# Kernel optimization log

Hardware: AMD Instinct MI355X
Metric: run time of the kernel (lower is better)

Reference implementation:

```python
import jax, jax.numpy as jnp
import numpy as np

N_NODES = 100000


def gcn_conv(x, edge_index, W, b, n_nodes):
    # PyG GCNConv: add self-loops, symmetric normalization D^-1/2 (A+I) D^-1/2, then XW + b
    xw = x @ W  # [N, out]
    loops = jnp.arange(n_nodes, dtype=edge_index.dtype)
    src = jnp.concatenate([edge_index[0], loops])  # [E+N]
    dst = jnp.concatenate([edge_index[1], loops])
    deg = jax.ops.segment_sum(jnp.ones_like(dst, dtype=xw.dtype), dst, num_segments=n_nodes)
    dinv = jnp.where(deg > 0, deg ** -0.5, 0.0).astype(xw.dtype)
    norm = dinv[src] * dinv[dst]  # [E+N]
    msgs = xw[src] * norm[:, None]  # gather source features, scale
    out = jax.ops.segment_sum(msgs, dst, num_segments=n_nodes)  # scatter-add at dst
    return out + b


def setup_inputs() -> dict:
    key = jax.random.key(0)
    k1, k2, k3, k4 = jax.random.split(key, 4)
    F_in, dim, n_cls, n_edges = 512, 32, 40, 3200000
    x = jax.random.normal(k1, (N_NODES, F_in), dtype=jnp.float32)
    edge_index = jax.random.randint(k2, (2, n_edges), 0, N_NODES, dtype=jnp.int64)
    W1 = jax.random.normal(k3, (F_in, dim), dtype=jnp.float32) * (1.0 / np.sqrt(F_in))
    b1 = jnp.zeros((dim,), dtype=jnp.float32)
    W2 = jax.random.normal(k4, (dim, n_cls), dtype=jnp.float32) * (1.0 / np.sqrt(dim))
    b2 = jnp.zeros((n_cls,), dtype=jnp.float32)
    return {"x": x, "edge_index": edge_index, "W1": W1, "b1": b1, "W2": W2, "b2": b2}


def reference(x, edge_index, W1, b1, W2, b2):
    h = jax.nn.relu(gcn_conv(x, edge_index, W1, b1, N_NODES))
    # F.dropout with training=False (eval) is identity
    logits = gcn_conv(h, edge_index, W2, b2, N_NODES)
    return jax.nn.log_softmax(logits, axis=1)
```

## Files before the change

### kernel.cpp

```cpp
#include <hip/hip_runtime.h>
#include <hip/hip_bf16.h>
#include <math.h>


#define DIM 32
#define NCLS 40
#define F_IN 512
#define BSH 8
#define EPB 8192
#define LMAX 9216

__device__ __forceinline__ unsigned int bf16rne(float x) {
    unsigned int u = __float_as_uint(x);
    return (u + 0x7fffu + ((u >> 16) & 1u)) >> 16;
}
__device__ __forceinline__ unsigned int packpair(float lo, float hi) {
    return bf16rne(lo) | (bf16rne(hi) << 16);
}
__device__ __forceinline__ void unpack8(uint4 u, float* f) {
    f[0] = __uint_as_float(u.x << 16);
    f[1] = __uint_as_float(u.x & 0xffff0000u);
    f[2] = __uint_as_float(u.y << 16);
    f[3] = __uint_as_float(u.y & 0xffff0000u);
    f[4] = __uint_as_float(u.z << 16);
    f[5] = __uint_as_float(u.z & 0xffff0000u);
    f[6] = __uint_as_float(u.w << 16);
    f[7] = __uint_as_float(u.w & 0xffff0000u);
}

__global__ __launch_bounds__(256) void hist_k(const int* __restrict__ dst,
                                              int* __restrict__ gh, int E, int nbk) {
    __shared__ int h[512];
    int tid = threadIdx.x;
    h[tid] = 0; h[tid + 256] = 0;
    __syncthreads();
    int base = blockIdx.x * EPB;
#pragma unroll 4
    for (int k = 0; k < EPB / 256; ++k) {
        int e = base + k * 256 + tid;
        if (e < E) atomicAdd(&h[dst[e] >> BSH], 1);
    }
    __syncthreads();
    if (h[tid]) atomicAdd(&gh[tid], h[tid]);
    if (h[tid + 256]) atomicAdd(&gh[tid + 256], h[tid + 256]);
}

__global__ __launch_bounds__(512) void scanb_k(const int* __restrict__ gh,
                                               int* __restrict__ bbase,
                                               int* __restrict__ gcur, int nbk) {
    __shared__ int sh[512];
    int t = threadIdx.x;
    int c = (t < nbk) ? gh[t] : 0;
    sh[t] = c;
    __syncthreads();
    for (int off = 1; off < 512; off <<= 1) {
        int v = sh[t];
        if (t >= off) v += sh[t - off];
        __syncthreads();
        sh[t] = v;
        __syncthreads();
    }
    int excl = sh[t] - c;
    if (t < nbk) { bbase[t] = excl; gcur[t] = excl; }
    if (t == 0) bbase[nbk] = sh[511];
}

__global__ __launch_bounds__(256) void part_k(const int* __restrict__ src,
                                              const int* __restrict__ dst,
                                              int* __restrict__ gcur,
                                              int* __restrict__ pairs, int E) {
    __shared__ int st[EPB];
    __shared__ int h[512];
    __shared__ int hb[512];
    int tid = threadIdx.x;
    h[tid] = 0; h[tid + 256] = 0;
    __syncthreads();
    int base = blockIdx.x * EPB;
#pragma unroll 4
    for (int k = 0; k < EPB / 256; ++k) {
        int e = base + k * 256 + tid;
        if (e < E) {
            int d = dst[e];
            st[k * 256 + tid] = d;
            atomicAdd(&h[d >> BSH], 1);
        }
    }
    __syncthreads();
    for (int b = tid; b < 512; b += 256) {
        int cnt = h[b];
        hb[b] = cnt ? atomicAdd(&gcur[b], cnt) : 0;
        h[b] = 0;
    }
    __syncthreads();
#pragma unroll 4
    for (int k = 0; k < EPB / 256; ++k) {
        int e = base + k * 256 + tid;
        if (e < E) {
            int d = st[k * 256 + tid];
            int b = d >> BSH;
            int r = atomicAdd(&h[b], 1);
            pairs[hb[b] + r] = ((d & 255) << 17) | src[e];
        }
    }
}

__global__ __launch_bounds__(256) void build_k(const int* __restrict__ pairs,
                                               const int* __restrict__ bbase,
                                               int* __restrict__ rowptr,
                                               int* __restrict__ csr,
                                               float* __restrict__ dinv,
                                               int n, int nbk, int E) {
    __shared__ int lcsr[LMAX];
    __shared__ int bins[256 * 17];
    __shared__ int cnt[256];
    __shared__ int sc[256];
    __shared__ int cur[256];
    int tid = threadIdx.x;
    int b = blockIdx.x;
    int lo = bbase[b], hi = bbase[b + 1];
    int cb = hi - lo; if (cb > LMAX) cb = LMAX;
    cnt[tid] = 0;
    __syncthreads();
    const int* Pb = pairs + lo;
    for (int i = tid; i < cb; i += 256)
        atomicAdd(&cnt[Pb[i] >> 17], 1);
    __syncthreads();
    int c = cnt[tid];
    sc[tid] = c;
    __syncthreads();
    for (int off = 1; off < 256; off <<= 1) {
        int v = sc[tid];
        if (tid >= off) v += sc[tid - off];
        __syncthreads();
        sc[tid] = v;
        __syncthreads();
    }
    int excl = sc[tid] - c;
    int v = (b << BSH) + tid;
    if (v < n) {
        rowptr[v] = lo + excl;
        dinv[v] = rsqrtf((float)(c + 1));
    }
    cur[tid] = excl;
    __syncthreads();
    for (int i = tid; i < cb; i += 256) {
        int p = Pb[i];
        int pos = atomicAdd(&cur[p >> 17], 1);
        lcsr[pos] = p & 0x1FFFF;
    }
    __syncthreads();
    {
        int* mb = &bins[tid * 17];
        int s = excl, e = excl + c;
#pragma unroll
        for (int k = 0; k < 16; ++k) mb[k] = 0;
        for (int i = s; i < e; ++i) ++mb[lcsr[i] >> 13];
        int run = s;
#pragma unroll
        for (int k = 0; k < 16; ++k) { int q = mb[k]; mb[k] = run; run += q; }
        for (int i = s; i < e; ++i) {
            int val = lcsr[i];
            int k = val >> 13;
            int pos = mb[k]++;
            csr[lo + pos] = val;
        }
    }
    if (b == 0 && tid == 0) rowptr[n] = E;
}

#define GR 128
__global__ __launch_bounds__(256) void gemm1_k(const float* __restrict__ x,
                                               const float* __restrict__ W1,
                                               const float* __restrict__ dinv,
                                               unsigned short* __restrict__ xwp, int n) {
    __shared__ float xs[32 * GR];
    __shared__ float ws[32 * 32];
    int tid = threadIdx.x;
    int base = blockIdx.x * GR;
    int rg = tid & 31;
    int cg = tid >> 5;
    float acc[4][4];
#pragma unroll
    for (int i = 0; i < 4; ++i)
#pragma unroll
        for (int j = 0; j < 4; ++j) acc[i][j] = 0.f;

    int lr = tid >> 1;
    int lq = tid & 1;
    int grow = base + lr;
    if (grow >= n) grow = n - 1;
    const float* xrow = x + (size_t)grow * F_IN;
    int wk = tid >> 3;
    int wc = tid & 7;

    for (int k0 = 0; k0 < F_IN; k0 += 32) {
        float4 a[4];
#pragma unroll
        for (int j = 0; j < 4; ++j)
            a[j] = *(const float4*)(xrow + k0 + lq * 16 + j * 4);
        float4 wv = *(const float4*)(W1 + (size_t)(k0 + wk) * DIM + wc * 4);
        __syncthreads();
#pragma unroll
        for (int j = 0; j < 4; ++j) {
            xs[(lq * 16 + j * 4 + 0) * GR + lr] = a[j].x;
            xs[(lq * 16 + j * 4 + 1) * GR + lr] = a[j].y;
            xs[(lq * 16 + j * 4 + 2) * GR + lr] = a[j].z;
            xs[(lq * 16 + j * 4 + 3) * GR + lr] = a[j].w;
        }
        *(float4*)&ws[wk * 32 + wc * 4] = wv;
        __syncthreads();
#pragma unroll 8
        for (int kk = 0; kk < 32; ++kk) {
            float4 xv = *(const float4*)&xs[kk * GR + rg * 4];
            float4 wv2 = *(const float4*)&ws[kk * 32 + cg * 4];
            acc[0][0] = fmaf(xv.x, wv2.x, acc[0][0]);
            acc[0][1] = fmaf(xv.x, wv2.y, acc[0][1]);
            acc[0][2] = fmaf(xv.x, wv2.z, acc[0][2]);
            acc[0][3] = fmaf(xv.x, wv2.w, acc[0][3]);
            acc[1][0] = fmaf(xv.y, wv2.x, acc[1][0]);
            acc[1][1] = fmaf(xv.y, wv2.y, acc[1][1]);
            acc[1][2] = fmaf(xv.y, wv2.z, acc[1][2]);
            acc[1][3] = fmaf(xv.y, wv2.w, acc[1][3]);
            acc[2][0] = fmaf(xv.z, wv2.x, acc[2][0]);
            acc[2][1] = fmaf(xv.z, wv2.y, acc[2][1]);
            acc[2][2] = fmaf(xv.z, wv2.z, acc[2][2]);
            acc[2][3] = fmaf(xv.z, wv2.w, acc[2][3]);
            acc[3][0] = fmaf(xv.w, wv2.x, acc[3][0]);
            acc[3][1] = fmaf(xv.w, wv2.y, acc[3][1]);
            acc[3][2] = fmaf(xv.w, wv2.z, acc[3][2]);
            acc[3][3] = fmaf(xv.w, wv2.w, acc[3][3]);
        }
    }
#pragma unroll
    for (int i = 0; i < 4; ++i) {
        int row = base + rg * 4 + i;
        if (row < n) {
            float dv = dinv[row];
            uint2 o;
            o.x = packpair(acc[i][0] * dv, acc[i][1] * dv);
            o.y = packpair(acc[i][2] * dv, acc[i][3] * dv);
            *(uint2*)(xwp + (size_t)row * DIM + cg * 4) = o;
        }
    }
}

__global__ __launch_bounds__(256) void agg1_k(const uint4* __restrict__ F,
                                              const int* __restrict__ rowptr,
                                              const int* __restrict__ csr,
                                              const float* __restrict__ dinv,
                                              const float* __restrict__ bias,
                                              uint4* __restrict__ out, int n) {
    int t = blockIdx.x * 256 + threadIdx.x;
    int v = t >> 2;
    int f8 = t & 3;
    if (v >= n) return;
    float s[8], tmp[8];
    unpack8(F[(size_t)v * 4 + f8], s);
    int e = rowptr[v];
    int end = rowptr[v + 1];
    for (; e + 3 < end; e += 4) {
        uint4 ua = F[(size_t)csr[e] * 4 + f8];
        uint4 ub = F[(size_t)csr[e + 1] * 4 + f8];
        uint4 uc = F[(size_t)csr[e + 2] * 4 + f8];
        uint4 ud = F[(size_t)csr[e + 3] * 4 + f8];
        unpack8(ua, tmp);
#pragma unroll
        for (int j = 0; j < 8; ++j) s[j] += tmp[j];
        unpack8(ub, tmp);
#pragma unroll
        for (int j = 0; j < 8; ++j) s[j] += tmp[j];
        unpack8(uc, tmp);
#pragma unroll
        for (int j = 0; j < 8; ++j) s[j] += tmp[j];
        unpack8(ud, tmp);
#pragma unroll
        for (int j = 0; j < 8; ++j) s[j] += tmp[j];
    }
    for (; e < end; ++e) {
        unpack8(F[(size_t)csr[e] * 4 + f8], tmp);
#pragma unroll
        for (int j = 0; j < 8; ++j) s[j] += tmp[j];
    }
    float dv = dinv[v];
    float4 b0 = *(const float4*)(bias + f8 * 8);
    float4 b1 = *(const float4*)(bias + f8 * 8 + 4);
    float bb[8] = {b0.x, b0.y, b0.z, b0.w, b1.x, b1.y, b1.z, b1.w};
    float r[8];
#pragma unroll
    for (int j = 0; j < 8; ++j) r[j] = fmaxf(s[j] * dv + bb[j], 0.f) * dv;
    uint4 o;
    o.x = packpair(r[0], r[1]);
    o.y = packpair(r[2], r[3]);
    o.z = packpair(r[4], r[5]);
    o.w = packpair(r[6], r[7]);
    out[(size_t)v * 4 + f8] = o;
}

__global__ __launch_bounds__(256) void agg2final_k(const uint4* __restrict__ F,
                                                   const int* __restrict__ rowptr,
                                                   const int* __restrict__ csr,
                                                   const float* __restrict__ dinv,
                                                   const float* __restrict__ W2,
                                                   const float* __restrict__ b2,
                                                   float* __restrict__ out, int n) {
    __shared__ float w2s[DIM * NCLS];
    __shared__ float b2s[NCLS];
    __shared__ float a2s[64 * 33];
    int tid = threadIdx.x;
    for (int i = tid; i < DIM * NCLS; i += 256) w2s[i] = W2[i];
    if (tid < NCLS) b2s[tid] = b2[tid];

    int nl = tid >> 2;
    int f8 = tid & 3;
    int v = blockIdx.x * 64 + nl;
    if (v < n) {
        float s[8], tmp[8];
        unpack8(F[(size_t)v * 4 + f8], s);
        int e = rowptr[v];
        int end = rowptr[v + 1];
        for (; e + 3 < end; e += 4) {
            uint4 ua = F[(size_t)csr[e] * 4 + f8];
            uint4 ub = F[(size_t)csr[e + 1] * 4 + f8];
            uint4 uc = F[(size_t)csr[e + 2] * 4 + f8];
            uint4 ud = F[(size_t)csr[e + 3] * 4 + f8];
            unpack8(ua, tmp);
#pragma unroll
            for (int j = 0; j < 8; ++j) s[j] += tmp[j];
            unpack8(ub, tmp);
#pragma unroll
            for (int j = 0; j < 8; ++j) s[j] += tmp[j];
            unpack8(uc, tmp);
#pragma unroll
            for (int j = 0; j < 8; ++j) s[j] += tmp[j];
            unpack8(ud, tmp);
#pragma unroll
            for (int j = 0; j < 8; ++j) s[j] += tmp[j];
        }
        for (; e < end; ++e) {
            unpack8(F[(size_t)csr[e] * 4 + f8], tmp);
#pragma unroll
            for (int j = 0; j < 8; ++j) s[j] += tmp[j];
        }
        float dv = dinv[v];
#pragma unroll
        for (int j = 0; j < 8; ++j) a2s[nl * 33 + f8 * 8 + j] = s[j] * dv;
    }
    __syncthreads();

    int q = f8;
    float lg[10];
#pragma unroll
    for (int c = 0; c < 10; ++c) lg[c] = b2s[q * 10 + c];
#pragma unroll
    for (int k = 0; k < DIM; ++k) {
        float a = a2s[nl * 33 + k];
        const float* wr = &w2s[k * NCLS + q * 10];
#pragma unroll
        for (int c = 0; c < 10; ++c) lg[c] += a * wr[c];
    }
    float m = lg[0];
#pragma unroll
    for (int c = 1; c < 10; ++c) m = fmaxf(m, lg[c]);
    m = fmaxf(m, __shfl_xor(m, 1));
    m = fmaxf(m, __shfl_xor(m, 2));
    float ssum = 0.f;
#pragma unroll
    for (int c = 0; c < 10; ++c) ssum += __expf(lg[c] - m);
    ssum += __shfl_xor(ssum, 1);
    ssum += __shfl_xor(ssum, 2);
    float lse = m + __logf(ssum);
    if (v < n) {
        float* o = out + (size_t)v * NCLS + q * 10;
#pragma unroll
        for (int c = 0; c < 10; ++c) o[c] = lg[c] - lse;
    }
}

extern "C" void kernel_launch(void* const* d_in, const int* in_sizes, int n_in,
                              void* d_out, int out_size, void* d_ws, size_t ws_size,
                              hipStream_t stream) {
    const float* x  = (const float*)d_in[0];
    const int*   ei = (const int*)d_in[1];
    const float* W1 = (const float*)d_in[2];
    const float* b1 = (const float*)d_in[3];
    const float* W2 = (const float*)d_in[4];
    const float* b2 = (const float*)d_in[5];
    float* out = (float*)d_out;

    int n = in_sizes[0] / F_IN;
    int E = in_sizes[1] / 2;
    const int* src = ei;
    const int* dst = ei + E;
    int nbk = (n + 255) >> BSH;

    char* w = (char*)d_ws;
    size_t off = 0;
    auto alloc = [&](size_t bytes) -> void* {
        void* p = w + off;
        off += (bytes + 255) & ~(size_t)255;
        return p;
    };
    size_t featB2 = ((size_t)n * DIM * 2 + 255) & ~(size_t)255;
    int*   csr    = (int*)alloc((size_t)E * 4);
    char*  pairsR = (char*)alloc((size_t)E * 4);
    int*   rowptr = (int*)alloc((size_t)(n + 1) * 4);
    float* dinv   = (float*)alloc((size_t)n * 4);
    int*   gh     = (int*)alloc(512 * 4);
    int*   bbase  = (int*)alloc(513 * 4);
    int*   gcur   = (int*)alloc(512 * 4);
    (void)ws_size;

    int*            pairs = (int*)pairsR;
    unsigned short* xwp   = (unsigned short*)pairsR;
    unsigned short* hts   = (unsigned short*)(pairsR + featB2);

    hipMemsetAsync(gh, 0, 512 * 4, stream);

    int nebk = (E + EPB - 1) / EPB;
    hist_k <<<nebk, 256, 0, stream>>>(dst, gh, E, nbk);
    scanb_k<<<1, 512, 0, stream>>>(gh, bbase, gcur, nbk);
    part_k <<<nebk, 256, 0, stream>>>(src, dst, gcur, pairs, E);
    build_k<<<nbk, 256, 0, stream>>>(pairs, bbase, rowptr, csr, dinv, n, nbk, E);

    gemm1_k<<<(n + GR - 1) / GR, 256, 0, stream>>>(x, W1, dinv, xwp, n);
    agg1_k<<<((size_t)n * 4 + 255) / 256, 256, 0, stream>>>(
        (const uint4*)xwp, rowptr, csr, dinv, b1, (uint4*)hts, n);
    agg2final_k<<<(n + 63) / 64, 256, 0, stream>>>(
        (const uint4*)hts, rowptr, csr, dinv, W2, b2, out, n);
}
```

Baseline: 512.7 us.

## Fuse edge partition and first GEMM into one launch, compute degree in histogram

Degrees are now counted with global atomics in the histogram pass, so dinv no longer depends on the CSR build. That lets the first-layer GEMM (x@W1 scaled by dinv) share a kernel launch with the edge-partition pass, using a shared-memory union and splitting blocks by blockIdx. Independent scatter work and dense GEMM can then overlap on the device. The cost is 3.2M extra global atomics on deg, an extra memset, a separate buffer for xwp instead of aliasing pairs, and rsqrt recomputed in the aggregation kernels.

```diff
diff --git a/kernel.cpp b/kernel.cpp
--- a/kernel.cpp
+++ b/kernel.cpp
@@ -1,5 +1,4 @@
 #include <hip/hip_runtime.h>
-#include <hip/hip_bf16.h>
 #include <math.h>
 
 
@@ -9,6 +8,7 @@
 #define BSH 8
 #define EPB 8192
 #define LMAX 9216
+#define GR 128
 
 __device__ __forceinline__ unsigned int bf16rne(float x) {
     unsigned int u = __float_as_uint(x);
@@ -28,8 +28,9 @@
     f[7] = __uint_as_float(u.w & 0xffff0000u);
 }
 
-__global__ __launch_bounds__(256) void hist_k(const int* __restrict__ dst,
-                                              int* __restrict__ gh, int E, int nbk) {
+__global__ __launch_bounds__(256) void histdeg_k(const int* __restrict__ dst,
+                                                 int* __restrict__ gh,
+                                                 int* __restrict__ deg, int E) {
     __shared__ int h[512];
     int tid = threadIdx.x;
     h[tid] = 0; h[tid + 256] = 0;
@@ -38,7 +39,11 @@
 #pragma unroll 4
     for (int k = 0; k < EPB / 256; ++k) {
         int e = base + k * 256 + tid;
-        if (e < E) atomicAdd(&h[dst[e] >> BSH], 1);
+        if (e < E) {
+            int d = dst[e];
+            atomicAdd(&h[d >> BSH], 1);
+            atomicAdd(&deg[d], 1);
+        }
     }
     __syncthreads();
     if (h[tid]) atomicAdd(&gh[tid], h[tid]);
@@ -65,41 +70,123 @@
     if (t == 0) bbase[nbk] = sh[511];
 }
 
-__global__ __launch_bounds__(256) void part_k(const int* __restrict__ src,
-                                              const int* __restrict__ dst,
-                                              int* __restrict__ gcur,
-                                              int* __restrict__ pairs, int E) {
-    __shared__ int st[EPB];
-    __shared__ int h[512];
-    __shared__ int hb[512];
+struct SmemPart { int st[EPB]; int h[512]; int hb[512]; };
+struct SmemGemm { float xs[32 * GR]; float ws[32 * 32]; };
+union SmemU { SmemPart p; SmemGemm g; };
+
+__global__ __launch_bounds__(256) void partgemm_k(const int* __restrict__ src,
+                                                  const int* __restrict__ dst,
+                                                  int* __restrict__ gcur,
+                                                  int* __restrict__ pairs, int E,
+                                                  const float* __restrict__ x,
+                                                  const float* __restrict__ W1,
+                                                  const int* __restrict__ deg,
+                                                  unsigned short* __restrict__ xwp,
+                                                  int n, int nebk) {
+    __shared__ SmemU u;
     int tid = threadIdx.x;
-    h[tid] = 0; h[tid + 256] = 0;
-    __syncthreads();
-    int base = blockIdx.x * EPB;
+
+    if ((int)blockIdx.x < nebk) {
+        int* st = u.p.st;
+        int* h  = u.p.h;
+        int* hb = u.p.hb;
+        h[tid] = 0; h[tid + 256] = 0;
+        __syncthreads();
+        int base = blockIdx.x * EPB;
 #pragma unroll 4
-    for (int k = 0; k < EPB / 256; ++k) {
-        int e = base + k * 256 + tid;
-        if (e < E) {
-            int d = dst[e];
-            st[k * 256 + tid] = d;
-            atomicAdd(&h[d >> BSH], 1);
-        }
-    }
-    __syncthreads();
-    for (int b = tid; b < 512; b += 256) {
-        int cnt = h[b];
-        hb[b] = cnt ? atomicAdd(&gcur[b], cnt) : 0;
-        h[b] = 0;
-    }
-    __syncthreads();
+        for (int k = 0; k < EPB / 256; ++k) {
+            int e = base + k * 256 + tid;
+            if (e < E) {
+                int d = dst[e];
+                st[k * 256 + tid] = d;
+                atomicAdd(&h[d >> BSH], 1);
+            }
+        }
+        __syncthreads();
+        for (int b = tid; b < 512; b += 256) {
+            int cnt = h[b];
+            hb[b] = cnt ? atomicAdd(&gcur[b], cnt) : 0;
+            h[b] = 0;
+        }
+        __syncthreads();
 #pragma unroll 4
-    for (int k = 0; k < EPB / 256; ++k) {
-        int e = base + k * 256 + tid;
-        if (e < E) {
-            int d = st[k * 256 + tid];
-            int b = d >> BSH;
-            int r = atomicAdd(&h[b], 1);
-            pairs[hb[b] + r] = ((d & 255) << 17) | src[e];
+        for (int k = 0; k < EPB / 256; ++k) {
+            int e = base + k * 256 + tid;
+            if (e < E) {
+                int d = st[k * 256 + tid];
+                int b = d >> BSH;
+                int r = atomicAdd(&h[b], 1);
+                pairs[hb[b] + r] = ((d & 255) << 17) | src[e];
+            }
+        }
+    } else {
+        float* xs = u.g.xs;
+        float* ws = u.g.ws;
+        int base = ((int)blockIdx.x - nebk) * GR;
+        int rg = tid & 31;
+        int cg = tid >> 5;
+        float acc[4][4];
+#pragma unroll
+        for (int i = 0; i < 4; ++i)
+#pragma unroll
+            for (int j = 0; j < 4; ++j) acc[i][j] = 0.f;
+
+        int lr = tid >> 1;
+        int lq = tid & 1;
+        int grow = base + lr;
+        if (grow >= n) grow = n - 1;
+        const float* xrow = x + (size_t)grow * F_IN;
+        int wk = tid >> 3;
+        int wc = tid & 7;
+
+        for (int k0 = 0; k0 < F_IN; k0 += 32) {
+            float4 a[4];
+#pragma unroll
+            for (int j = 0; j < 4; ++j)
+                a[j] = *(const float4*)(xrow + k0 + lq * 16 + j * 4);
+            float4 wv = *(const float4*)(W1 + (size_t)(k0 + wk) * DIM + wc * 4);
+            __syncthreads();
+#pragma unroll
+            for (int j = 0; j < 4; ++j) {
+                xs[(lq * 16 + j * 4 + 0) * GR + lr] = a[j].x;
+                xs[(lq * 16 + j * 4 + 1) * GR + lr] = a[j].y;
+                xs[(lq * 16 + j * 4 + 2) * GR + lr] = a[j].z;
+                xs[(lq * 16 + j * 4 + 3) * GR + lr] = a[j].w;
+            }
+            *(float4*)&ws[wk * 32 + wc * 4] = wv;
+            __syncthreads();
+#pragma unroll 8
+            for (int kk = 0; kk < 32; ++kk) {
+                float4 xv  = *(const float4*)&xs[kk * GR + rg * 4];
+                float4 wv2 = *(const float4*)&ws[kk * 32 + cg * 4];
+                acc[0][0] = fmaf(xv.x, wv2.x, acc[0][0]);
+                acc[0][1] = fmaf(xv.x, wv2.y, acc[0][1]);
+                acc[0][2] = fmaf(xv.x, wv2.z, acc[0][2]);
+                acc[0][3] = fmaf(xv.x, wv2.w, acc[0][3]);
+                acc[1][0] = fmaf(xv.y, wv2.x, acc[1][0]);
+                acc[1][1] = fmaf(xv.y, wv2.y, acc[1][1]);
+                acc[1][2] = fmaf(xv.y, wv2.z, acc[1][2]);
+                acc[1][3] = fmaf(xv.y, wv2.w, acc[1][3]);
+                acc[2][0] = fmaf(xv.z, wv2.x, acc[2][0]);
+                acc[2][1] = fmaf(xv.z, wv2.y, acc[2][1]);
+                acc[2][2] = fmaf(xv.z, wv2.z, acc[2][2]);
+                acc[2][3] = fmaf(xv.z, wv2.w, acc[2][3]);
+                acc[3][0] = fmaf(xv.w, wv2.x, acc[3][0]);
+                acc[3][1] = fmaf(xv.w, wv2.y, acc[3][1]);
+                acc[3][2] = fmaf(xv.w, wv2.z, acc[3][2]);
+                acc[3][3] = fmaf(xv.w, wv2.w, acc[3][3]);
+            }
+        }
+#pragma unroll
+        for (int i = 0; i < 4; ++i) {
+            int row = base + rg * 4 + i;
+            if (row < n) {
+                float dv = rsqrtf((float)deg[row] + 1.0f);
+                uint2 o;
+                o.x = packpair(acc[i][0] * dv, acc[i][1] * dv);
+                o.y = packpair(acc[i][2] * dv, acc[i][3] * dv);
+                *(uint2*)(xwp + (size_t)row * DIM + cg * 4) = o;
+            }
         }
     }
 }
@@ -108,7 +195,6 @@
                                                const int* __restrict__ bbase,
                                                int* __restrict__ rowptr,
                                                int* __restrict__ csr,
-                                               float* __restrict__ dinv,
                                                int n, int nbk, int E) {
     __shared__ int lcsr[LMAX];
     __shared__ int bins[256 * 17];
@@ -137,10 +223,7 @@
     }
     int excl = sc[tid] - c;
     int v = (b << BSH) + tid;
-    if (v < n) {
-        rowptr[v] = lo + excl;
-        dinv[v] = rsqrtf((float)(c + 1));
-    }
+    if (v < n) rowptr[v] = lo + excl;
     cur[tid] = excl;
     __syncthreads();
     for (int i = tid; i < cb; i += 256) {
@@ -168,86 +251,10 @@
     if (b == 0 && tid == 0) rowptr[n] = E;
 }
 
-#define GR 128
-__global__ __launch_bounds__(256) void gemm1_k(const float* __restrict__ x,
-                                               const float* __restrict__ W1,
-                                               const float* __restrict__ dinv,
-                                               unsigned short* __restrict__ xwp, int n) {
-    __shared__ float xs[32 * GR];
-    __shared__ float ws[32 * 32];
-    int tid = threadIdx.x;
-    int base = blockIdx.x * GR;
-    int rg = tid & 31;
-    int cg = tid >> 5;
-    float acc[4][4];
-#pragma unroll
-    for (int i = 0; i < 4; ++i)
-#pragma unroll
-        for (int j = 0; j < 4; ++j) acc[i][j] = 0.f;
-
-    int lr = tid >> 1;
-    int lq = tid & 1;
-    int grow = base + lr;
-    if (grow >= n) grow = n - 1;
-    const float* xrow = x + (size_t)grow * F_IN;
-    int wk = tid >> 3;
-    int wc = tid & 7;
-
-    for (int k0 = 0; k0 < F_IN; k0 += 32) {
-        float4 a[4];
-#pragma unroll
-        for (int j = 0; j < 4; ++j)
-            a[j] = *(const float4*)(xrow + k0 + lq * 16 + j * 4);
-        float4 wv = *(const float4*)(W1 + (size_t)(k0 + wk) * DIM + wc * 4);
-        __syncthreads();
-#pragma unroll
-        for (int j = 0; j < 4; ++j) {
-            xs[(lq * 16 + j * 4 + 0) * GR + lr] = a[j].x;
-            xs[(lq * 16 + j * 4 + 1) * GR + lr] = a[j].y;
-            xs[(lq * 16 + j * 4 + 2) * GR + lr] = a[j].z;
-            xs[(lq * 16 + j * 4 + 3) * GR + lr] = a[j].w;
-        }
-        *(float4*)&ws[wk * 32 + wc * 4] = wv;
-        __syncthreads();
-#pragma unroll 8
-        for (int kk = 0; kk < 32; ++kk) {
-            float4 xv = *(const float4*)&xs[kk * GR + rg * 4];
-            float4 wv2 = *(const float4*)&ws[kk * 32 + cg * 4];
-            acc[0][0] = fmaf(xv.x, wv2.x, acc[0][0]);
-            acc[0][1] = fmaf(xv.x, wv2.y, acc[0][1]);
-            acc[0][2] = fmaf(xv.x, wv2.z, acc[0][2]);
-            acc[0][3] = fmaf(xv.x, wv2.w, acc[0][3]);
-            acc[1][0] = fmaf(xv.y, wv2.x, acc[1][0]);
-            acc[1][1] = fmaf(xv.y, wv2.y, acc[1][1]);
-            acc[1][2] = fmaf(xv.y, wv2.z, acc[1][2]);
-            acc[1][3] = fmaf(xv.y, wv2.w, acc[1][3]);
-            acc[2][0] = fmaf(xv.z, wv2.x, acc[2][0]);
-            acc[2][1] = fmaf(xv.z, wv2.y, acc[2][1]);
-            acc[2][2] = fmaf(xv.z, wv2.z, acc[2][2]);
-            acc[2][3] = fmaf(xv.z, wv2.w, acc[2][3]);
-            acc[3][0] = fmaf(xv.w, wv2.x, acc[3][0]);
-            acc[3][1] = fmaf(xv.w, wv2.y, acc[3][1]);
-            acc[3][2] = fmaf(xv.w, wv2.z, acc[3][2]);
-            acc[3][3] = fmaf(xv.w, wv2.w, acc[3][3]);
-        }
-    }
-#pragma unroll
-    for (int i = 0; i < 4; ++i) {
-        int row = base + rg * 4 + i;
-        if (row < n) {
-            float dv = dinv[row];
-            uint2 o;
-            o.x = packpair(acc[i][0] * dv, acc[i][1] * dv);
-            o.y = packpair(acc[i][2] * dv, acc[i][3] * dv);
-            *(uint2*)(xwp + (size_t)row * DIM + cg * 4) = o;
-        }
-    }
-}
-
 __global__ __launch_bounds__(256) void agg1_k(const uint4* __restrict__ F,
                                               const int* __restrict__ rowptr,
                                               const int* __restrict__ csr,
-                                              const float* __restrict__ dinv,
+                                              const int* __restrict__ deg,
                                               const float* __restrict__ bias,
                                               uint4* __restrict__ out, int n) {
     int t = blockIdx.x * 256 + threadIdx.x;
@@ -281,7 +288,7 @@
 #pragma unroll
         for (int j = 0; j < 8; ++j) s[j] += tmp[j];
     }
-    float dv = dinv[v];
+    float dv = rsqrtf((float)deg[v] + 1.0f);
     float4 b0 = *(const float4*)(bias + f8 * 8);
     float4 b1 = *(const float4*)(bias + f8 * 8 + 4);
     float bb[8] = {b0.x, b0.y, b0.z, b0.w, b1.x, b1.y, b1.z, b1.w};
@@ -299,7 +306,7 @@
 __global__ __launch_bounds__(256) void agg2final_k(const uint4* __restrict__ F,
                                                    const int* __restrict__ rowptr,
                                                    const int* __restrict__ csr,
-                                                   const float* __restrict__ dinv,
+                                                   const int* __restrict__ deg,
                                                    const float* __restrict__ W2,
                                                    const float* __restrict__ b2,
                                                    float* __restrict__ out, int n) {
@@ -341,7 +348,7 @@
 #pragma unroll
             for (int j = 0; j < 8; ++j) s[j] += tmp[j];
         }
-        float dv = dinv[v];
+        float dv = rsqrtf((float)deg[v] + 1.0f);
 #pragma unroll
         for (int j = 0; j < 8; ++j) a2s[nl * 33 + f8 * 8 + j] = s[j] * dv;
     }
@@ -403,28 +410,31 @@
     size_t featB2 = ((size_t)n * DIM * 2 + 255) & ~(size_t)255;
     int*   csr    = (int*)alloc((size_t)E * 4);
     char*  pairsR = (char*)alloc((size_t)E * 4);
+    unsigned short* xwp = (unsigned short*)alloc(featB2);
     int*   rowptr = (int*)alloc((size_t)(n + 1) * 4);
-    float* dinv   = (float*)alloc((size_t)n * 4);
+    int*   deg    = (int*)alloc((size_t)n * 4);
     int*   gh     = (int*)alloc(512 * 4);
     int*   bbase  = (int*)alloc(513 * 4);
     int*   gcur   = (int*)alloc(512 * 4);
     (void)ws_size;
 
     int*            pairs = (int*)pairsR;
-    unsigned short* xwp   = (unsigned short*)pairsR;
-    unsigned short* hts   = (unsigned short*)(pairsR + featB2);
+    unsigned short* hts   = (unsigned short*)pairsR;
 
     hipMemsetAsync(gh, 0, 512 * 4, stream);
+    hipMemsetAsync(deg, 0, (size_t)n * 4, stream);
 
     int nebk = (E + EPB - 1) / EPB;
-    hist_k <<<nebk, 256, 0, stream>>>(dst, gh, E, nbk);
-    scanb_k<<<1, 512, 0, stream>>>(gh, bbase, gcur, nbk);
-    part_k <<<nebk, 256, 0, stream>>>(src, dst, gcur, pairs, E);
-    build_k<<<nbk, 256, 0, stream>>>(pairs, bbase, rowptr, csr, dinv, n, nbk, E);
-
-    gemm1_k<<<(n + GR - 1) / GR, 256, 0, stream>>>(x, W1, dinv, xwp, n);
+    int ngm  = (n + GR - 1) / GR;
+
+    histdeg_k<<<nebk, 256, 0, stream>>>(dst, gh, deg, E);
+    scanb_k  <<<1, 512, 0, stream>>>(gh, bbase, gcur, nbk);
+    partgemm_k<<<nebk + ngm, 256, 0, stream>>>(src, dst, gcur, pairs, E,
+                                               x, W1, deg, xwp, n, nebk);
+    build_k  <<<nbk, 256, 0, stream>>>(pairs, bbase, rowptr, csr, n, nbk, E);
+
     agg1_k<<<((size_t)n * 4 + 255) / 256, 256, 0, stream>>>(
-        (const uint4*)xwp, rowptr, csr, dinv, b1, (uint4*)hts, n);
+        (const uint4*)xwp, rowptr, csr, deg, b1, (uint4*)hts, n);
     agg2final_k<<<(n + 63) / 64, 256, 0, stream>>>(
-        (const uint4*)hts, rowptr, csr, dinv, W2, b2, out, n);
-}
+        (const uint4*)hts, rowptr, csr, deg, W2, b2, out, n);
+}
```

Result: slower. 610.5 us (+19.1%).
